# Kernel optimization log

Measured on AMD Instinct MI355X. Metric: run time of the kernel, lower is better.

The kernel has to match this reference:

```python
import jax, jax.numpy as jnp
import numpy as np


def _gru_cell(xi, h, w_ih, w_hh, b_ih, b_hh):
    # Faithful torch.nn.GRUCell math (as written in KeyedGRU.get_key_gate.one_step)
    gi = xi @ w_ih.T + b_ih            # [B, 3H]
    gh = h @ w_hh.T + b_hh             # [B, 3H]
    i_r, i_i, i_n = jnp.split(gi, 3, axis=1)
    h_r, h_i, h_n = jnp.split(gh, 3, axis=1)
    resetgate = jax.nn.sigmoid(i_r + h_r)
    inputgate = jax.nn.sigmoid(i_i + h_i)
    newgate = jnp.tanh(i_n + resetgate * h_n)
    hy = newgate + inputgate * (h - newgate)
    return hy, resetgate


def setup_inputs() -> dict:
    key = jax.random.key(0)
    ks = jax.random.split(key, 6)
    B, T, I, H = 64, 2048, 256, 256
    KB, KL = 4, 16
    s = 1.0 / float(np.sqrt(H))
    x = jax.random.normal(ks[0], (B, T, I), jnp.float32)
    wm_key = jax.random.normal(ks[1], (KB, KL, I), jnp.float32)
    weight_ih = jax.random.uniform(ks[2], (3 * H, I), jnp.float32, -s, s)
    weight_hh = jax.random.uniform(ks[3], (3 * H, H), jnp.float32, -s, s)
    bias_ih = jax.random.uniform(ks[4], (3 * H,), jnp.float32, -s, s)
    bias_hh = jax.random.uniform(ks[5], (3 * H,), jnp.float32, -s, s)
    return {"x": x, "wm_key": wm_key, "weight_ih": weight_ih,
            "weight_hh": weight_hh, "bias_ih": bias_ih, "bias_hh": bias_hh}


def reference(x, wm_key, weight_ih, weight_hh, bias_ih, bias_hh):
    B, T, I = x.shape
    H = weight_hh.shape[1]
    dt = x.dtype

    # --- key-gate scan (get_key_gate): collect reset gate per key timestep ---
    kt = jnp.transpose(wm_key, (1, 0, 2))          # [KL, KB, I]
    KL, KB, _ = kt.shape
    kh0 = jnp.zeros((KB, H), dt)                   # hidden_init='zero'

    def kstep(h, xi):
        hy, r = _gru_cell(xi, h, weight_ih, weight_hh, bias_ih, bias_hh)
        return hy, r

    _, rgates = jax.lax.scan(kstep, kh0, kt)       # [KL, KB, H]
    gate_means = rgates.mean(axis=1)               # [KL, H] -- key_gates[i].mean(dim=0)
    # pad with ones for steps i >= key_len (no gating applied there)
    gates_full = jnp.concatenate([gate_means, jnp.ones((T - KL, H), dt)], axis=0)  # [T, H]

    # --- main recurrence (teacher_forcing=True, return_sequences=True) ---
    xt = jnp.transpose(x, (1, 0, 2))               # [T, B, I]
    h0 = jnp.zeros((B, H), dt)

    def step(h, inp):
        xi, g = inp
        hy, _ = _gru_cell(xi, h, weight_ih, weight_hh, bias_ih, bias_hh)
        # NOTE: original appends hy to output BEFORE the key-gate multiply,
        # but carries the gated hidden state forward.
        return hy * g, hy

    _, out = jax.lax.scan(step, h0, (xt, gates_full))  # out: [T, B, H]
    return out
```

## Files before the change

### kernel.cpp

```cpp
#include <hip/hip_runtime.h>

typedef _Float16 f16;
typedef _Float16 half8 __attribute__((ext_vector_type(8)));
typedef _Float16 half2v __attribute__((ext_vector_type(2)));
typedef _Float16 half4 __attribute__((ext_vector_type(4)));
typedef float f32x4 __attribute__((ext_vector_type(4)));
typedef unsigned int uint2v __attribute__((ext_vector_type(2)));

#define G3 768

__global__ void cvt_f32_f16(const float* __restrict__ in, f16* __restrict__ out, int n) {
  int i = blockIdx.x * blockDim.x + threadIdx.x;
  if (i < n) out[i] = (f16)in[i];
}

__global__ __launch_bounds__(256, 2)
void gi_gemm(const float* __restrict__ A, const f16* __restrict__ W,
             const float* __restrict__ b_ih, const float* __restrict__ b_hh,
             f16* __restrict__ GIri, f16* __restrict__ GIn) {
  const int tid = threadIdx.x;
  const int lane = tid & 63;
  const int w = tid >> 6;
  const int quad = lane >> 4;
  const int lq = lane & 15;
  const int m0 = blockIdx.x * 64;

  __shared__ __align__(16) f16 Al[64 * 264];
  __shared__ __align__(16) f16 Bl[48 * 264];

#pragma unroll
  for (int i = 0; i < 16; ++i) {
    int f = i * 256 + tid;
    int row = f >> 6;
    int c4 = f & 63;
    float4 v = ((const float4*)A)[(size_t)(m0 + row) * 64 + c4];
    half4 hv = {(f16)v.x, (f16)v.y, (f16)v.z, (f16)v.w};
    *(half4*)&Al[row * 264 + c4 * 4] = hv;
  }
  __syncthreads();

  half8 af[8];
#pragma unroll
  for (int kc = 0; kc < 8; ++kc)
    af[kc] = *(half8*)&Al[(w * 16 + lq) * 264 + kc * 32 + quad * 8];

  for (int nc = 0; nc < 16; ++nc) {
    __syncthreads();
    int n0 = nc * 48;
#pragma unroll
    for (int i = 0; i < 6; ++i) {
      int f = i * 256 + tid;
      int row = f >> 5;
      int c8 = f & 31;
      half8 v = ((const half8*)(W + (size_t)(n0 + row) * 256))[c8];
      *(half8*)&Bl[row * 264 + c8 * 8] = v;
    }
    __syncthreads();

    f32x4 acc[3] = {};
#pragma unroll
    for (int kc = 0; kc < 8; ++kc) {
#pragma unroll
      for (int nt = 0; nt < 3; ++nt) {
        half8 bf = *(half8*)&Bl[(nt * 16 + lq) * 264 + kc * 32 + quad * 8];
        acc[nt] = __builtin_amdgcn_mfma_f32_16x16x32_f16(af[kc], bf, acc[nt], 0, 0, 0);
      }
    }
#pragma unroll
    for (int nt = 0; nt < 3; ++nt) {
      int n = n0 + nt * 16 + lq;
      float bv = b_ih[n] + (n < 512 ? b_hh[n] : 0.f);
      int g = n >> 8;
      int u = n & 255;
      int ww = u >> 5, lq16 = u & 15, s = (u >> 4) & 1;
#pragma unroll
      for (int r = 0; r < 4; ++r) {
        int m = m0 + w * 16 + quad * 4 + r;
        float val = acc[nt][r] + bv;
        size_t base = ((size_t)m * 8 + ww) * 16 + lq16;
        if (g < 2) GIri[base * 4 + g * 2 + s] = (f16)val;
        else       GIn[base * 2 + s] = (f16)val;
      }
    }
  }
}

__device__ __forceinline__ float sigf(float x) {
  return __builtin_amdgcn_rcpf(1.f + __expf(-x));
}
__device__ __forceinline__ float tanhf_(float x) {
  return 1.f - 2.f * __builtin_amdgcn_rcpf(__expf(2.f * x) + 1.f);
}

#define MF(af, bw, c) __builtin_amdgcn_mfma_f32_16x16x32_f16(af, bw, c, 0, 0, 0)

#define KC_ALL(af, kc) \
  a0 = MF(af, w0##kc, a0); a1 = MF(af, w1##kc, a1); a2 = MF(af, w2##kc, a2); \
  a3 = MF(af, w3##kc, a3); a4 = MF(af, w4##kc, a4); a5 = MF(af, w5##kc, a5);

#define LOADW(t6, kc) { \
    const float* wr_ = Whh + (size_t)(((t6 >> 1) * 256) + w * 32 + ((t6 & 1) * 16) + lq) * 256 + (kc * 32 + colb); \
    float4 va_ = *(const float4*)wr_; float4 vb_ = *(const float4*)(wr_ + 4); \
    w##t6##kc = (half8){(f16)va_.x, (f16)va_.y, (f16)va_.z, (f16)va_.w, \
                        (f16)vb_.x, (f16)vb_.y, (f16)vb_.z, (f16)vb_.w}; }

#define LOADW_T6(t6) \
  LOADW(t6, 0) LOADW(t6, 1) LOADW(t6, 2) LOADW(t6, 3) \
  LOADW(t6, 4) LOADW(t6, 5) LOADW(t6, 6) LOADW(t6, 7)

#define UNPACK2(u32, lo, hi) { half2v h2_ = __builtin_bit_cast(half2v, (unsigned int)(u32)); \
                               lo = (float)h2_[0]; hi = (float)h2_[1]; }

#define STEP(tcur, PRI, PN) { \
    const f16* hr_ = &hbuf[(tcur) & 1][0]; \
    f32x4 a0 = {}, a1 = {}, a2 = {}, a3 = {}, a4 = {}, a5 = {}; \
    half8 f0_ = *(const half8*)(hr_ + 0 * 32 + colb); \
    half8 f1_ = *(const half8*)(hr_ + 1 * 32 + colb); \
    half8 f2_ = *(const half8*)(hr_ + 2 * 32 + colb); \
    half8 f3_ = *(const half8*)(hr_ + 3 * 32 + colb); \
    KC_ALL(f0_, 0) \
    half8 f4_ = *(const half8*)(hr_ + 4 * 32 + colb); \
    KC_ALL(f1_, 1) \
    half8 f5_ = *(const half8*)(hr_ + 5 * 32 + colb); \
    KC_ALL(f2_, 2) \
    half8 f6_ = *(const half8*)(hr_ + 6 * 32 + colb); \
    KC_ALL(f3_, 3) \
    half8 f7_ = *(const half8*)(hr_ + 7 * 32 + colb); \
    KC_ALL(f4_, 4) KC_ALL(f5_, 5) KC_ALL(f6_, 6) KC_ALL(f7_, 7) \
    float gr0_, gr1_, gi0_, gi1_, gn0_, gn1_; \
    UNPACK2(PRI[0], gr0_, gr1_); \
    UNPACK2(PRI[1], gi0_, gi1_); \
    UNPACK2(PN, gn0_, gn1_); \
    if ((tcur) + 2 < T) { \
      PRI = *(const uint2v*)(gri + (size_t)((tcur) + 2) * 512); \
      PN = *(const unsigned int*)(gn + (size_t)((tcur) + 2) * 256); \
    } \
    float rg0_ = sigf(gr0_ + a0[0]); \
    float rg1_ = sigf(gr1_ + a1[0]); \
    float ig0_ = sigf(gi0_ + a2[0]); \
    float ig1_ = sigf(gi1_ + a3[0]); \
    float ng0_ = tanhf_(gn0_ + rg0_ * (bn0 + a4[0])); \
    float ng1_ = tanhf_(gn1_ + rg1_ * (bn1 + a5[0])); \
    float hy0_ = ng0_ + ig0_ * (h0 - ng0_); \
    float hy1_ = ng1_ + ig1_ * (h1 - ng1_); \
    if (IS_KEY) { \
      if (quad == 0) { float* o_ = out + ((size_t)(tcur) * nb + b) * 256 + u0; o_[0] = rg0_; o_[16] = rg1_; } \
      h0 = hy0_; h1 = hy1_; \
    } else { \
      if (quad == 0) { float* o_ = out + ((size_t)(tcur) * nb + b) * 256 + u0; o_[0] = hy0_; o_[16] = hy1_; } \
      float gm0_ = 1.f, gm1_ = 1.f; \
      if ((tcur) < 16) { gm0_ = gates[(tcur) * 256 + u0]; gm1_ = gates[(tcur) * 256 + u0 + 16]; } \
      h0 = hy0_ * gm0_; h1 = hy1_ * gm1_; \
    } \
    if (quad == 0) { f16* hw_ = &hbuf[((tcur) + 1) & 1][0]; hw_[u0] = (f16)h0; hw_[u0 + 16] = (f16)h1; } \
    __asm__ volatile("" ::: "memory"); \
    __builtin_amdgcn_s_waitcnt(0xC07F);  \
    __builtin_amdgcn_s_barrier(); \
    __asm__ volatile("" ::: "memory"); }

template <bool IS_KEY>
__global__ __launch_bounds__(512)
__attribute__((amdgpu_waves_per_eu(2, 2)))
void gru_scan(const float* __restrict__ Whh, const float* __restrict__ bhh,
              const f16* __restrict__ GIri, const f16* __restrict__ GIn,
              const float* __restrict__ gates, float* __restrict__ out, int T) {
  const int tid = threadIdx.x;
  const int lane = tid & 63;
  const int w = tid >> 6;
  const int quad = lane >> 4;
  const int lq = lane & 15;
  const int b = blockIdx.x;
  const int nb = gridDim.x;
  const int colb = quad * 8;
  const int u0 = w * 32 + lq;

  __shared__ __align__(16) f16 hbuf[2][256];

  half8 w00, w01, w02, w03, w04, w05, w06, w07;
  half8 w10, w11, w12, w13, w14, w15, w16, w17;
  half8 w20, w21, w22, w23, w24, w25, w26, w27;
  half8 w30, w31, w32, w33, w34, w35, w36, w37;
  half8 w40, w41, w42, w43, w44, w45, w46, w47;
  half8 w50, w51, w52, w53, w54, w55, w56, w57;
  LOADW_T6(0) LOADW_T6(1) LOADW_T6(2) LOADW_T6(3) LOADW_T6(4) LOADW_T6(5)

  if (tid < 256) { hbuf[0][tid] = (f16)0.f; hbuf[1][tid] = (f16)0.f; }

  float h0 = 0.f, h1 = 0.f;
  const float bn0 = bhh[512 + u0];
  const float bn1 = bhh[512 + u0 + 16];

  const size_t mstart = (size_t)b * T;
  const f16* gri = GIri + ((mstart * 8 + w) * 16 + lq) * 4;
  const f16* gn  = GIn + ((mstart * 8 + w) * 16 + lq) * 2;

  uint2v priA = *(const uint2v*)(gri);
  unsigned int pnA = *(const unsigned int*)(gn);
  uint2v priB = *(const uint2v*)(gri + 512);
  unsigned int pnB = *(const unsigned int*)(gn + 256);

  __syncthreads();

  for (int t = 0; t < T; t += 2) {
    STEP(t, priA, pnA)
    STEP(t + 1, priB, pnB)
  }
}

__global__ void gate_mean(const float* __restrict__ rg, float* __restrict__ g) {
  int i = blockIdx.x * 256 + threadIdx.x;
  int l = i >> 8;
  int j = i & 255;
  float s = 0.f;
#pragma unroll
  for (int kb = 0; kb < 4; ++kb) s += rg[((size_t)l * 4 + kb) * 256 + j];
  g[i] = 0.25f * s;
}

extern "C" void kernel_launch(void* const* d_in, const int* in_sizes, int n_in,
                              void* d_out, int out_size, void* d_ws, size_t ws_size,
                              hipStream_t stream) {
  const float* x      = (const float*)d_in[0];
  const float* wm_key = (const float*)d_in[1];
  const float* w_ih   = (const float*)d_in[2];
  const float* w_hh   = (const float*)d_in[3];
  const float* b_ih   = (const float*)d_in[4];
  const float* b_hh   = (const float*)d_in[5];
  float* out = (float*)d_out;

  char* ws = (char*)d_ws;
  const size_t GIRI_OFF  = 0;
  const size_t GIN_OFF   = GIRI_OFF + 134217728ull;
  const size_t WIH_OFF   = GIN_OFF + 67108864ull;
  const size_t GIKRI_OFF = WIH_OFF + 393216ull;
  const size_t GIKN_OFF  = GIKRI_OFF + 65536ull;
  const size_t RG_OFF    = GIKN_OFF + 32768ull;
  const size_t G_OFF     = RG_OFF + 65536ull;
  f16*   GIri  = (f16*)(ws + GIRI_OFF);
  f16*   GIn   = (f16*)(ws + GIN_OFF);
  f16*   Wih   = (f16*)(ws + WIH_OFF);
  f16*   GIkri = (f16*)(ws + GIKRI_OFF);
  f16*   GIkn  = (f16*)(ws + GIKN_OFF);
  float* rg    = (float*)(ws + RG_OFF);
  float* g     = (float*)(ws + G_OFF);

  cvt_f32_f16<<<dim3(768), dim3(256), 0, stream>>>(w_ih, Wih, G3 * 256);
  gi_gemm<<<dim3(2048), dim3(256), 0, stream>>>(x, Wih, b_ih, b_hh, GIri, GIn);
  gi_gemm<<<dim3(1), dim3(256), 0, stream>>>(wm_key, Wih, b_ih, b_hh, GIkri, GIkn);
  gru_scan<true><<<dim3(4), dim3(512), 0, stream>>>(w_hh, b_hh, GIkri, GIkn, g, rg, 16);
  gate_mean<<<dim3(16), dim3(256), 0, stream>>>(rg, g);
  gru_scan<false><<<dim3(64), dim3(512), 0, stream>>>(w_hh, b_hh, GIri, GIn, g, out, 2048);
}
```

Before: 3.014 ms.

## Replace MFMA recurrent matvec with packed fdot2 dot products and cross-lane reductions

The per-step h·W_hh product, which padded a single hidden-state row into 16x16 MFMA tiles, is replaced with packed f16 fdot2 dot products. Each lane holds a contiguous 64-element slice of six weight rows in registers. Partial sums are combined across the four quads with a ds_swizzle and a ds_bpermute. The hidden state is stored to LDS in a permuted layout so each lane reads its contiguous slice. This avoids MFMA work wasted on 15 empty rows, at the cost of more VALU instructions and cross-lane reduction latency on the serial critical path.

```diff
diff --git a/kernel.cpp b/kernel.cpp
--- a/kernel.cpp
+++ b/kernel.cpp
@@ -92,41 +92,49 @@
   return 1.f - 2.f * __builtin_amdgcn_rcpf(__expf(2.f * x) + 1.f);
 }
 
-#define MF(af, bw, c) __builtin_amdgcn_mfma_f32_16x16x32_f16(af, bw, c, 0, 0, 0)
-
-#define KC_ALL(af, kc) \
-  a0 = MF(af, w0##kc, a0); a1 = MF(af, w1##kc, a1); a2 = MF(af, w2##kc, a2); \
-  a3 = MF(af, w3##kc, a3); a4 = MF(af, w4##kc, a4); a5 = MF(af, w5##kc, a5);
-
-#define LOADW(t6, kc) { \
-    const float* wr_ = Whh + (size_t)(((t6 >> 1) * 256) + w * 32 + ((t6 & 1) * 16) + lq) * 256 + (kc * 32 + colb); \
-    float4 va_ = *(const float4*)wr_; float4 vb_ = *(const float4*)(wr_ + 4); \
-    w##t6##kc = (half8){(f16)va_.x, (f16)va_.y, (f16)va_.z, (f16)va_.w, \
-                        (f16)vb_.x, (f16)vb_.y, (f16)vb_.z, (f16)vb_.w}; }
-
-#define LOADW_T6(t6) \
-  LOADW(t6, 0) LOADW(t6, 1) LOADW(t6, 2) LOADW(t6, 3) \
-  LOADW(t6, 4) LOADW(t6, 5) LOADW(t6, 6) LOADW(t6, 7)
+#if defined(__has_builtin)
+#if __has_builtin(__builtin_amdgcn_fdot2)
+#define FD(a, b, c) __builtin_amdgcn_fdot2(a, b, c, false)
+#endif
+#endif
+#ifndef FD
+#define FD(a, b, c) ((c) + (float)(a)[0] * (float)(b)[0] + (float)(a)[1] * (float)(b)[1])
+#endif
 
 #define UNPACK2(u32, lo, hi) { half2v h2_ = __builtin_bit_cast(half2v, (unsigned int)(u32)); \
                                lo = (float)h2_[0]; hi = (float)h2_[1]; }
 
+#define LW(arr, g, u) { \
+    const float* p_ = Whh + ((size_t)(g) * 256 + (u)) * 256 + quad * 64; \
+    _Pragma("unroll") \
+    for (int c_ = 0; c_ < 16; ++c_) { \
+      float4 v_ = ((const float4*)p_)[c_]; \
+      arr[c_ * 2]     = (half2v){(f16)v_.x, (f16)v_.y}; \
+      arr[c_ * 2 + 1] = (half2v){(f16)v_.z, (f16)v_.w}; \
+    } }
+
+#define D6(h2, j) \
+  ar0 = FD(h2, wr0[j], ar0); ar1 = FD(h2, wr1[j], ar1); \
+  ai0 = FD(h2, wi0[j], ai0); ai1 = FD(h2, wi1[j], ai1); \
+  an0 = FD(h2, wn0[j], an0); an1 = FD(h2, wn1[j], an1);
+
+#define DCHUNK(c) { \
+    half8 hv_ = *(const half8*)(hr_ + (c) * 32 + colb); \
+    { half2v h2_ = (half2v){hv_[0], hv_[1]}; D6(h2_, (c) * 4 + 0) } \
+    { half2v h2_ = (half2v){hv_[2], hv_[3]}; D6(h2_, (c) * 4 + 1) } \
+    { half2v h2_ = (half2v){hv_[4], hv_[5]}; D6(h2_, (c) * 4 + 2) } \
+    { half2v h2_ = (half2v){hv_[6], hv_[7]}; D6(h2_, (c) * 4 + 3) } }
+
+#define RED(x) { \
+    int t_ = __builtin_amdgcn_ds_swizzle(__builtin_bit_cast(int, x), 0x401F); \
+    x += __builtin_bit_cast(float, t_); \
+    t_ = __builtin_amdgcn_ds_bpermute(pidx, __builtin_bit_cast(int, x)); \
+    x += __builtin_bit_cast(float, t_); }
+
 #define STEP(tcur, PRI, PN) { \
     const f16* hr_ = &hbuf[(tcur) & 1][0]; \
-    f32x4 a0 = {}, a1 = {}, a2 = {}, a3 = {}, a4 = {}, a5 = {}; \
-    half8 f0_ = *(const half8*)(hr_ + 0 * 32 + colb); \
-    half8 f1_ = *(const half8*)(hr_ + 1 * 32 + colb); \
-    half8 f2_ = *(const half8*)(hr_ + 2 * 32 + colb); \
-    half8 f3_ = *(const half8*)(hr_ + 3 * 32 + colb); \
-    KC_ALL(f0_, 0) \
-    half8 f4_ = *(const half8*)(hr_ + 4 * 32 + colb); \
-    KC_ALL(f1_, 1) \
-    half8 f5_ = *(const half8*)(hr_ + 5 * 32 + colb); \
-    KC_ALL(f2_, 2) \
-    half8 f6_ = *(const half8*)(hr_ + 6 * 32 + colb); \
-    KC_ALL(f3_, 3) \
-    half8 f7_ = *(const half8*)(hr_ + 7 * 32 + colb); \
-    KC_ALL(f4_, 4) KC_ALL(f5_, 5) KC_ALL(f6_, 6) KC_ALL(f7_, 7) \
+    float ar0 = 0.f, ar1 = 0.f, ai0 = 0.f, ai1 = 0.f, an0 = 0.f, an1 = 0.f; \
+    DCHUNK(0) DCHUNK(1) DCHUNK(2) DCHUNK(3) \
     float gr0_, gr1_, gi0_, gi1_, gn0_, gn1_; \
     UNPACK2(PRI[0], gr0_, gr1_); \
     UNPACK2(PRI[1], gi0_, gi1_); \
@@ -135,12 +143,14 @@
       PRI = *(const uint2v*)(gri + (size_t)((tcur) + 2) * 512); \
       PN = *(const unsigned int*)(gn + (size_t)((tcur) + 2) * 256); \
     } \
-    float rg0_ = sigf(gr0_ + a0[0]); \
-    float rg1_ = sigf(gr1_ + a1[0]); \
-    float ig0_ = sigf(gi0_ + a2[0]); \
-    float ig1_ = sigf(gi1_ + a3[0]); \
-    float ng0_ = tanhf_(gn0_ + rg0_ * (bn0 + a4[0])); \
-    float ng1_ = tanhf_(gn1_ + rg1_ * (bn1 + a5[0])); \
+    DCHUNK(4) DCHUNK(5) DCHUNK(6) DCHUNK(7) \
+    RED(ar0) RED(ar1) RED(an0) RED(an1) RED(ai0) RED(ai1) \
+    float rg0_ = sigf(gr0_ + ar0); \
+    float rg1_ = sigf(gr1_ + ar1); \
+    float ig0_ = sigf(gi0_ + ai0); \
+    float ig1_ = sigf(gi1_ + ai1); \
+    float ng0_ = tanhf_(gn0_ + rg0_ * (bn0 + an0)); \
+    float ng1_ = tanhf_(gn1_ + rg1_ * (bn1 + an1)); \
     float hy0_ = ng0_ + ig0_ * (h0 - ng0_); \
     float hy1_ = ng1_ + ig1_ * (h1 - ng1_); \
     if (IS_KEY) { \
@@ -152,7 +162,7 @@
       if ((tcur) < 16) { gm0_ = gates[(tcur) * 256 + u0]; gm1_ = gates[(tcur) * 256 + u0 + 16]; } \
       h0 = hy0_ * gm0_; h1 = hy1_ * gm1_; \
     } \
-    if (quad == 0) { f16* hw_ = &hbuf[((tcur) + 1) & 1][0]; hw_[u0] = (f16)h0; hw_[u0 + 16] = (f16)h1; } \
+    if (quad == 0) { f16* hw_ = &hbuf[((tcur) + 1) & 1][0]; hw_[wa0] = (f16)h0; hw_[wa1] = (f16)h1; } \
     __asm__ volatile("" ::: "memory"); \
     __builtin_amdgcn_s_waitcnt(0xC07F);  \
     __builtin_amdgcn_s_barrier(); \
@@ -173,22 +183,24 @@
   const int nb = gridDim.x;
   const int colb = quad * 8;
   const int u0 = w * 32 + lq;
+  const int pidx = (lane ^ 32) << 2;
 
   __shared__ __align__(16) f16 hbuf[2][256];
 
-  half8 w00, w01, w02, w03, w04, w05, w06, w07;
-  half8 w10, w11, w12, w13, w14, w15, w16, w17;
-  half8 w20, w21, w22, w23, w24, w25, w26, w27;
-  half8 w30, w31, w32, w33, w34, w35, w36, w37;
-  half8 w40, w41, w42, w43, w44, w45, w46, w47;
-  half8 w50, w51, w52, w53, w54, w55, w56, w57;
-  LOADW_T6(0) LOADW_T6(1) LOADW_T6(2) LOADW_T6(3) LOADW_T6(4) LOADW_T6(5)
-
-  if (tid < 256) { hbuf[0][tid] = (f16)0.f; hbuf[1][tid] = (f16)0.f; }
+  const int u1 = u0 + 16;
+  const int wa0 = ((u0 & 63) >> 3) * 32 + (u0 >> 6) * 8 + (u0 & 7);
+  const int wa1 = ((u1 & 63) >> 3) * 32 + (u1 >> 6) * 8 + (u1 & 7);
+
+  half2v wr0[32], wr1[32], wi0[32], wi1[32], wn0[32], wn1[32];
+  LW(wr0, 0, u0) LW(wr1, 0, u1)
+  LW(wi0, 1, u0) LW(wi1, 1, u1)
+  LW(wn0, 2, u0) LW(wn1, 2, u1)
+
+  if (tid < 256) { ((f16*)hbuf)[tid] = (f16)0.f; ((f16*)hbuf)[256 + tid] = (f16)0.f; }
 
   float h0 = 0.f, h1 = 0.f;
   const float bn0 = bhh[512 + u0];
-  const float bn1 = bhh[512 + u0 + 16];
+  const float bn1 = bhh[512 + u1];
 
   const size_t mstart = (size_t)b * T;
   const f16* gri = GIri + ((mstart * 8 + w) * 16 + lq) * 4;
```

After: 3.131 ms. +3.9%, slower.

## Move n-gate hidden weights to LDS and compute via fdot2 with cross-lane reduction

Applied to the files above, without the earlier changes.

The n-gate third of W_hh is no longer held in registers as MFMA B-fragments. It is converted once to fp16 into a 128KB XOR-swizzled LDS array. Each step computes the n-gate dot products with packed fdot2 instructions reading that LDS, then reduces across quads with ds_swizzle and bpermute. This cuts MFMA count per step from 48 to 32 and frees register pressure, at the cost of extra LDS traffic, VALU work and a cross-lane reduction on the serial critical path.

```diff
diff --git a/kernel.cpp b/kernel.cpp
--- a/kernel.cpp
+++ b/kernel.cpp
@@ -6,6 +6,7 @@
 typedef _Float16 half4 __attribute__((ext_vector_type(4)));
 typedef float f32x4 __attribute__((ext_vector_type(4)));
 typedef unsigned int uint2v __attribute__((ext_vector_type(2)));
+typedef unsigned int u32x4v __attribute__((ext_vector_type(4)));
 
 #define G3 768
 
@@ -92,11 +93,16 @@
   return 1.f - 2.f * __builtin_amdgcn_rcpf(__expf(2.f * x) + 1.f);
 }
 
+#if defined(__has_builtin)
+#if __has_builtin(__builtin_amdgcn_fdot2)
+#define FD(a, b, c) __builtin_amdgcn_fdot2(a, b, c, false)
+#endif
+#endif
+#ifndef FD
+#define FD(a, b, c) ((c) + (float)(a)[0] * (float)(b)[0] + (float)(a)[1] * (float)(b)[1])
+#endif
+
 #define MF(af, bw, c) __builtin_amdgcn_mfma_f32_16x16x32_f16(af, bw, c, 0, 0, 0)
-
-#define KC_ALL(af, kc) \
-  a0 = MF(af, w0##kc, a0); a1 = MF(af, w1##kc, a1); a2 = MF(af, w2##kc, a2); \
-  a3 = MF(af, w3##kc, a3); a4 = MF(af, w4##kc, a4); a5 = MF(af, w5##kc, a5);
 
 #define LOADW(t6, kc) { \
     const float* wr_ = Whh + (size_t)(((t6 >> 1) * 256) + w * 32 + ((t6 & 1) * 16) + lq) * 256 + (kc * 32 + colb); \
@@ -111,22 +117,38 @@
 #define UNPACK2(u32, lo, hi) { half2v h2_ = __builtin_bit_cast(half2v, (unsigned int)(u32)); \
                                lo = (float)h2_[0]; hi = (float)h2_[1]; }
 
+#define H2(v4, j) __builtin_bit_cast(half2v, (unsigned int)((v4)[j]))
+
+#define NCHUNK(c) { \
+    a0 = MF(f##c##_, w0##c, a0); a1 = MF(f##c##_, w1##c, a1); \
+    a2 = MF(f##c##_, w2##c, a2); a3 = MF(f##c##_, w3##c, a3); \
+    int no_ = nC0 ^ ((c) << 6); \
+    half8 n0_ = *(const half8*)((const char*)n_lds + no_); \
+    half8 n1_ = *(const half8*)((const char*)n_lds + no_ + 8192); \
+    u32x4v hu_ = __builtin_bit_cast(u32x4v, f##c##_); \
+    u32x4v nu0_ = __builtin_bit_cast(u32x4v, n0_); \
+    u32x4v nu1_ = __builtin_bit_cast(u32x4v, n1_); \
+    an0 = FD(H2(hu_, 0), H2(nu0_, 0), an0); an1 = FD(H2(hu_, 0), H2(nu1_, 0), an1); \
+    an0 = FD(H2(hu_, 1), H2(nu0_, 1), an0); an1 = FD(H2(hu_, 1), H2(nu1_, 1), an1); \
+    an0 = FD(H2(hu_, 2), H2(nu0_, 2), an0); an1 = FD(H2(hu_, 2), H2(nu1_, 2), an1); \
+    an0 = FD(H2(hu_, 3), H2(nu0_, 3), an0); an1 = FD(H2(hu_, 3), H2(nu1_, 3), an1); }
+
+#define RED(x) { \
+    int t_ = __builtin_amdgcn_ds_swizzle(__builtin_bit_cast(int, x), 0x401F); \
+    x += __builtin_bit_cast(float, t_); \
+    t_ = __builtin_amdgcn_ds_bpermute(pidx, __builtin_bit_cast(int, x)); \
+    x += __builtin_bit_cast(float, t_); }
+
 #define STEP(tcur, PRI, PN) { \
     const f16* hr_ = &hbuf[(tcur) & 1][0]; \
-    f32x4 a0 = {}, a1 = {}, a2 = {}, a3 = {}, a4 = {}, a5 = {}; \
     half8 f0_ = *(const half8*)(hr_ + 0 * 32 + colb); \
     half8 f1_ = *(const half8*)(hr_ + 1 * 32 + colb); \
     half8 f2_ = *(const half8*)(hr_ + 2 * 32 + colb); \
     half8 f3_ = *(const half8*)(hr_ + 3 * 32 + colb); \
-    KC_ALL(f0_, 0) \
     half8 f4_ = *(const half8*)(hr_ + 4 * 32 + colb); \
-    KC_ALL(f1_, 1) \
     half8 f5_ = *(const half8*)(hr_ + 5 * 32 + colb); \
-    KC_ALL(f2_, 2) \
     half8 f6_ = *(const half8*)(hr_ + 6 * 32 + colb); \
-    KC_ALL(f3_, 3) \
     half8 f7_ = *(const half8*)(hr_ + 7 * 32 + colb); \
-    KC_ALL(f4_, 4) KC_ALL(f5_, 5) KC_ALL(f6_, 6) KC_ALL(f7_, 7) \
     float gr0_, gr1_, gi0_, gi1_, gn0_, gn1_; \
     UNPACK2(PRI[0], gr0_, gr1_); \
     UNPACK2(PRI[1], gi0_, gi1_); \
@@ -135,12 +157,17 @@
       PRI = *(const uint2v*)(gri + (size_t)((tcur) + 2) * 512); \
       PN = *(const unsigned int*)(gn + (size_t)((tcur) + 2) * 256); \
     } \
+    f32x4 a0 = {}, a1 = {}, a2 = {}, a3 = {}; \
+    float an0 = 0.f, an1 = 0.f; \
+    NCHUNK(0) NCHUNK(1) NCHUNK(2) NCHUNK(3) \
+    NCHUNK(4) NCHUNK(5) NCHUNK(6) NCHUNK(7) \
+    RED(an0) RED(an1) \
     float rg0_ = sigf(gr0_ + a0[0]); \
     float rg1_ = sigf(gr1_ + a1[0]); \
     float ig0_ = sigf(gi0_ + a2[0]); \
     float ig1_ = sigf(gi1_ + a3[0]); \
-    float ng0_ = tanhf_(gn0_ + rg0_ * (bn0 + a4[0])); \
-    float ng1_ = tanhf_(gn1_ + rg1_ * (bn1 + a5[0])); \
+    float ng0_ = tanhf_(gn0_ + rg0_ * (bn0 + an0)); \
+    float ng1_ = tanhf_(gn1_ + rg1_ * (bn1 + an1)); \
     float hy0_ = ng0_ + ig0_ * (h0 - ng0_); \
     float hy1_ = ng1_ + ig1_ * (h1 - ng1_); \
     if (IS_KEY) { \
@@ -173,18 +200,33 @@
   const int nb = gridDim.x;
   const int colb = quad * 8;
   const int u0 = w * 32 + lq;
-
+  const int pidx = (lane ^ 32) << 2;
+
+  __shared__ __align__(16) f16 n_lds[256 * 256];
   __shared__ __align__(16) f16 hbuf[2][256];
 
   half8 w00, w01, w02, w03, w04, w05, w06, w07;
   half8 w10, w11, w12, w13, w14, w15, w16, w17;
   half8 w20, w21, w22, w23, w24, w25, w26, w27;
   half8 w30, w31, w32, w33, w34, w35, w36, w37;
-  half8 w40, w41, w42, w43, w44, w45, w46, w47;
-  half8 w50, w51, w52, w53, w54, w55, w56, w57;
-  LOADW_T6(0) LOADW_T6(1) LOADW_T6(2) LOADW_T6(3) LOADW_T6(4) LOADW_T6(5)
+  LOADW_T6(0) LOADW_T6(1) LOADW_T6(2) LOADW_T6(3)
+
+#pragma unroll 4
+  for (int i = 0; i < 16; ++i) {
+    int gid = i * 512 + tid;
+    int rn = gid >> 5, g = gid & 31;
+    const float* p_ = Whh + (size_t)(512 + rn) * 256 + g * 8;
+    float4 va = *(const float4*)p_;
+    float4 vb = *(const float4*)(p_ + 4);
+    half8 hv = {(f16)va.x, (f16)va.y, (f16)va.z, (f16)va.w,
+                (f16)vb.x, (f16)vb.y, (f16)vb.z, (f16)vb.w};
+    *(half8*)((char*)n_lds + rn * 512 + ((g ^ (rn & 7)) << 4)) = hv;
+  }
 
   if (tid < 256) { hbuf[0][tid] = (f16)0.f; hbuf[1][tid] = (f16)0.f; }
+
+  const int e_ = u0 & 7;
+  const int nC0 = u0 * 512 + ((quad ^ (e_ & 3)) << 4) + ((e_ >> 2) << 6);
 
   float h0 = 0.f, h1 = 0.f;
   const float bn0 = bhh[512 + u0];
```

After: 3.503 ms. 16.2% more time.
